# Kernel tuning notes

Measured on AMD Instinct MI355X. Metric: run time of the kernel, lower is better.

Reference implementation:

```python
import jax
import jax.numpy as jnp
import numpy as np

# Config mirroring GLOBAL_CONFIG['attn'] / kernel config in the source
BM = 64            # query-group (block) size; asserted 64 or 192 in source
TOP_KEYS = 0.1     # fraction of keys kept via top-k on colsum scores
MULTIPLE_OF = 64   # counts_multiple_of: indices_count rounded to this
LW1D = 0.15        # local_1d_window fraction
RAND_INV_PROB = 100

B, H, N, D = 1, 12, 2048, 128


def setup_inputs() -> dict:
    key = jax.random.key(0)
    kq, kk, kv, kc = jax.random.split(key, 4)
    shape = (B, H, N, D)
    q = jax.random.normal(kq, shape, dtype=jnp.float32)
    k = jax.random.normal(kk, shape, dtype=jnp.float32)
    v = jax.random.normal(kv, shape, dtype=jnp.float32)
    out_cache = jax.random.normal(kc, shape, dtype=jnp.float32)
    return {"q": q, "k": k, "v": v, "out_cache": out_cache}


def _static_1d_mask(n: int, bm: int, lw1d: float) -> jnp.ndarray:
    # initialize_1d_static_mask: per query-group local window centered at
    # qg*bm + bm//2, width int(lw1d*n), clipped to [0, n). Shape [qg, n].
    qg = n // bm
    ws = int(lw1d * n)
    centers = jnp.arange(qg) * bm + bm // 2          # [qg]
    j = jnp.arange(n)                                  # [n]
    lo = centers[:, None] - ws // 2
    hi = centers[:, None] + ws // 2
    return (j[None, :] >= lo) & (j[None, :] < hi)


def _scatter_true(mask, idx):
    # mask.scatter_(-1, idx, True) along last axis
    K = idx.shape[-1]
    n = mask.shape[-1]
    flat = mask.reshape(-1, n)
    fidx = idx.reshape(-1, K)
    rows = jnp.arange(flat.shape[0])[:, None]
    flat = flat.at[rows, fidx].set(True)
    return flat.reshape(mask.shape)


def _sparse_diff_attn(q, k, v, out_cache):
    b, h, n, d = q.shape
    qg = n // BM
    scale = 1.0 / jnp.sqrt(jnp.asarray(d, q.dtype))
    # dense scores (dense_colsum_attn computes these on the full step)
    scores = jnp.einsum('bhid,bhjd->bhij', q, k) * scale   # [b,h,n,n]
    probs = jax.nn.softmax(scores, axis=-1)
    # bs: column-sum of attention probabilities per query group  [b,h,qg,n]
    bs = probs.reshape(b, h, qg, BM, n).sum(axis=3)
    # indices_count = multiple_of * round(top_keys * n / multiple_of)
    indices_count = MULTIPLE_OF * int(round(TOP_KEYS * n / MULTIPLE_OF))
    rmask = jax.random.randint(jax.random.key(1), bs.shape, 0, RAND_INV_PROB) == 0
    _, idx = jax.lax.top_k(bs, indices_count)
    mask = _scatter_true(rmask, idx)                       # [b,h,qg,n]
    static = _static_1d_mask(n, BM, LW1D)                  # [qg,n]
    # video_query_groups: groups where static window + topk still sparse
    vqg = (static.sum(axis=-1, keepdims=True) + indices_count) < n  # [qg,1]
    mask = mask & vqg[None, None]
    mask = mask | static[None, None]
    # csp_attn: block-sparse attention; every query i in group i//BM attends
    # only to keys selected in mask[.., i//BM, :]
    full_mask = jnp.repeat(mask, BM, axis=2)               # [b,h,n,n]
    sp_scores = jnp.where(full_mask, scores, -jnp.inf)
    sp_probs = jax.nn.softmax(sp_scores, axis=-1)
    sp_out = jnp.einsum('bhij,bhjd->bhid', sp_probs, v)
    # sparse step: o = o_cache + csp_attn(...)  (sign = +1)
    return out_cache + sp_out


def reference(q, k, v, out_cache):
    return _sparse_diff_attn(q, k, v, out_cache)
```

## Files before the change

kernel.cpp:

```cpp
#include <hip/hip_runtime.h>
#include <math.h>

constexpr int Hh   = 12;
constexpr int Nn   = 2048;
constexpr int Dd   = 128;
constexpr int BMq  = 64;
constexpr int QGg  = 32;
constexpr int KSEL = 192;
constexpr int CK   = 32;
constexpr float SCALE = 0.08838834764831845f;

typedef _Float16 v8h __attribute__((ext_vector_type(8)));
typedef float    v4f __attribute__((ext_vector_type(4)));

__device__ __attribute__((aligned(16))) _Float16 g_qh[(size_t)Hh*Nn*Dd];
__device__ __attribute__((aligned(16))) _Float16 g_ql[(size_t)Hh*Nn*Dd];
__device__ __attribute__((aligned(16))) _Float16 g_kh[(size_t)Hh*Nn*Dd];
__device__ __attribute__((aligned(16))) _Float16 g_kl[(size_t)Hh*Nn*Dd];
__device__ float          g_lp[(size_t)Hh*Nn*16];
__device__ float          g_bs[(size_t)Hh*QGg*Nn];
__device__ unsigned short g_sel[Hh*QGg*Nn];
__device__ int            g_cnt[Hh*QGg];

__device__ __forceinline__ unsigned int rotl32(unsigned int x, int n){
  return (x << n) | (x >> (32 - n));
}

__device__ __forceinline__ unsigned pack2h(_Float16 a, _Float16 b){
  unsigned short ua, ub;
  __builtin_memcpy(&ua, &a, 2);
  __builtin_memcpy(&ub, &b, 2);
  return (unsigned)ua | ((unsigned)ub << 16);
}

__device__ __forceinline__ void tf2x32(unsigned int k0, unsigned int k1,
                                       unsigned int x0, unsigned int x1,
                                       unsigned int &o0, unsigned int &o1){
  const unsigned int ks2 = 0x1BD11BDAu ^ k0 ^ k1;
  x0 += k0; x1 += k1;
  x0 += x1; x1 = rotl32(x1,13); x1 ^= x0;
  x0 += x1; x1 = rotl32(x1,15); x1 ^= x0;
  x0 += x1; x1 = rotl32(x1,26); x1 ^= x0;
  x0 += x1; x1 = rotl32(x1, 6); x1 ^= x0;
  x0 += k1; x1 += ks2 + 1u;
  x0 += x1; x1 = rotl32(x1,17); x1 ^= x0;
  x0 += x1; x1 = rotl32(x1,29); x1 ^= x0;
  x0 += x1; x1 = rotl32(x1,16); x1 ^= x0;
  x0 += x1; x1 = rotl32(x1,24); x1 ^= x0;
  x0 += ks2; x1 += k0 + 2u;
  x0 += x1; x1 = rotl32(x1,13); x1 ^= x0;
  x0 += x1; x1 = rotl32(x1,15); x1 ^= x0;
  x0 += x1; x1 = rotl32(x1,26); x1 ^= x0;
  x0 += x1; x1 = rotl32(x1, 6); x1 ^= x0;
  x0 += k0; x1 += k1 + 3u;
  x0 += x1; x1 = rotl32(x1,17); x1 ^= x0;
  x0 += x1; x1 = rotl32(x1,29); x1 ^= x0;
  x0 += x1; x1 = rotl32(x1,16); x1 ^= x0;
  x0 += x1; x1 = rotl32(x1,24); x1 ^= x0;
  x0 += k1; x1 += ks2 + 4u;
  x0 += x1; x1 = rotl32(x1,13); x1 ^= x0;
  x0 += x1; x1 = rotl32(x1,15); x1 ^= x0;
  x0 += x1; x1 = rotl32(x1,26); x1 ^= x0;
  x0 += x1; x1 = rotl32(x1, 6); x1 ^= x0;
  x0 += ks2; x1 += k0 + 5u;
  o0 = x0; o1 = x1;
}

__device__ __forceinline__ bool jax_rand01(unsigned int idx,
                                           unsigned int k1a, unsigned int k1b,
                                           unsigned int k2a, unsigned int k2b){
  unsigned int h0, h1, l0, l1;
  tf2x32(k1a, k1b, 0u, idx, h0, h1);
  tf2x32(k2a, k2b, 0u, idx, l0, l1);
  unsigned int h = h0 ^ h1;
  unsigned int l = l0 ^ l1;
  unsigned int off = ((h % 100u) * 96u + (l % 100u)) % 100u;
  return off == 0u;
}

__global__ __launch_bounds__(256) void k0_cvt(const float* __restrict__ Q,
                                              const float* __restrict__ K){
  const int bid = blockIdx.x;
  const int t = threadIdx.x;
  const int kc = t >> 6, ln = t & 63;
  const int row = ln & 15;
  const int col = kc*32 + (ln >> 4)*8;
  const size_t src = ((size_t)bid*16 + row)*Dd + col;
  const size_t ob  = (((size_t)bid)*4 + kc)*512 + (size_t)ln*8;

  float4 qa = *(const float4*)(Q + src);
  float4 qb = *(const float4*)(Q + src + 4);
  float qs[8] = {qa.x*SCALE, qa.y*SCALE, qa.z*SCALE, qa.w*SCALE,
                 qb.x*SCALE, qb.y*SCALE, qb.z*SCALE, qb.w*SCALE};
  v8h qh, ql;
  #pragma unroll
  for (int j = 0; j < 8; ++j){
    _Float16 hi = (_Float16)qs[j];
    qh[j] = hi;
    ql[j] = (_Float16)(qs[j] - (float)hi);
  }
  *(v8h*)&g_qh[ob] = qh;
  *(v8h*)&g_ql[ob] = ql;

  float4 ka = *(const float4*)(K + src);
  float4 kb = *(const float4*)(K + src + 4);
  float ks[8] = {ka.x, ka.y, ka.z, ka.w, kb.x, kb.y, kb.z, kb.w};
  v8h kh, kl;
  #pragma unroll
  for (int j = 0; j < 8; ++j){
    _Float16 hi = (_Float16)ks[j];
    kh[j] = hi;
    kl[j] = (_Float16)(ks[j] - (float)hi);
  }
  *(v8h*)&g_kh[ob] = kh;
  *(v8h*)&g_kl[ob] = kl;
}

__global__ __launch_bounds__(256) void k1_rowsum(){
  const int bid0 = blockIdx.x;
  const int w = (bid0 & 7)*384 + (bid0 >> 3);
  const int jb = w & 15, gp = (w >> 4) & 15, h = w >> 8;
  const int t = threadIdx.x;
  const int wv = t >> 6, ln = t & 63;
  const int nidx = ln & 15, quad = ln >> 4;
  const size_t lnoff = (size_t)ln*8;
  const size_t habase = ((size_t)h*128 + gp*8 + wv*2)*4;
  const size_t hbbase = ((size_t)h*128 + jb*8)*4;

  __shared__ v8h Bh[2][8][64], Bl[2][8][64];
  const int f0 = t*2, f1 = t*2 + 1;
  const int tc0 = f0 >> 6, bln0 = f0 & 63;
  const int tc1 = f1 >> 6, bln1 = f1 & 63;

  v8h rbh0, rbh1, rbl0, rbl1;
  {
    const size_t a0 = (hbbase + tc0*4 + 0)*512 + (size_t)bln0*8;
    const size_t a1 = (hbbase + tc1*4 + 0)*512 + (size_t)bln1*8;
    rbh0 = *(const v8h*)&g_kh[a0]; rbh1 = *(const v8h*)&g_kh[a1];
    rbl0 = *(const v8h*)&g_kl[a0]; rbl1 = *(const v8h*)&g_kl[a1];
  }

  v4f acc[2][8];
  #pragma unroll
  for (int tr = 0; tr < 2; ++tr)
    #pragma unroll
    for (int tc = 0; tc < 8; ++tc)
      acc[tr][tc] = (v4f){0.f, 0.f, 0.f, 0.f};

  for (int kc = 0; kc < 4; ++kc){
    const int cur = kc & 1;
    Bh[cur][tc0][bln0] = rbh0; Bh[cur][tc1][bln1] = rbh1;
    Bl[cur][tc0][bln0] = rbl0; Bl[cur][tc1][bln1] = rbl1;
    __syncthreads();
    if (kc < 3){
      const size_t a0 = (hbbase + tc0*4 + kc+1)*512 + (size_t)bln0*8;
      const size_t a1 = (hbbase + tc1*4 + kc+1)*512 + (size_t)bln1*8;
      rbh0 = *(const v8h*)&g_kh[a0]; rbh1 = *(const v8h*)&g_kh[a1];
      rbl0 = *(const v8h*)&g_kl[a0]; rbl1 = *(const v8h*)&g_kl[a1];
    }
    v8h ahi[2], alo[2];
    #pragma unroll
    for (int tr = 0; tr < 2; ++tr){
      const size_t ab = (habase + tr*4 + kc)*512 + lnoff;
      ahi[tr] = *(const v8h*)&g_qh[ab];
      alo[tr] = *(const v8h*)&g_ql[ab];
    }
    #pragma unroll
    for (int tc = 0; tc < 8; ++tc){
      v8h bh = Bh[cur][tc][ln];
      v8h bl = Bl[cur][tc][ln];
      #pragma unroll
      for (int tr = 0; tr < 2; ++tr){
        acc[tr][tc] = __builtin_amdgcn_mfma_f32_16x16x32_f16(ahi[tr], bh, acc[tr][tc], 0, 0, 0);
        acc[tr][tc] = __builtin_amdgcn_mfma_f32_16x16x32_f16(ahi[tr], bl, acc[tr][tc], 0, 0, 0);
        acc[tr][tc] = __builtin_amdgcn_mfma_f32_16x16x32_f16(alo[tr], bh, acc[tr][tc], 0, 0, 0);
      }
    }
  }

  #pragma unroll
  for (int tr = 0; tr < 2; ++tr){
    float rs[4] = {0.f, 0.f, 0.f, 0.f};
    #pragma unroll
    for (int tc = 0; tc < 8; ++tc){
      #pragma unroll
      for (int r = 0; r < 4; ++r){
        rs[r] += __expf(acc[tr][tc][r]);
      }
    }
    #pragma unroll
    for (int r = 0; r < 4; ++r){
      float v = rs[r];
      v += __shfl_xor(v, 1);
      v += __shfl_xor(v, 2);
      v += __shfl_xor(v, 4);
      v += __shfl_xor(v, 8);
      rs[r] = v;
    }
    if (nidx == 0){
      #pragma unroll
      for (int r = 0; r < 4; ++r){
        const int row = (wv*2+tr)*16 + quad*4 + r;
        g_lp[((size_t)h*Nn + gp*128 + row)*16 + jb] = rs[r];
      }
    }
  }
}

__global__ __launch_bounds__(256) void k2r_colsum(){
  const int bid0 = blockIdx.x;
  const int w = (bid0 & 7)*384 + (bid0 >> 3);
  const int jb = w & 15, gp = (w >> 4) & 15, h = w >> 8;
  const int t = threadIdx.x;
  const int wv = t >> 6, ln = t & 63;
  const int nidx = ln & 15, quad = ln >> 4;
  const size_t lnoff = (size_t)ln*8;
  const size_t habase = ((size_t)h*128 + gp*8 + wv*2)*4;
  const size_t hbbase = ((size_t)h*128 + jb*8)*4;

  __shared__ v8h Bh[2][8][64], Bl[2][8][64];
  __shared__ float il_s[128];
  __shared__ float part[4][128];
  const int f0 = t*2, f1 = t*2 + 1;
  const int tc0 = f0 >> 6, bln0 = f0 & 63;
  const int tc1 = f1 >> 6, bln1 = f1 & 63;

  v8h rbh0, rbh1, rbl0, rbl1;
  {
    const size_t a0 = (hbbase + tc0*4 + 0)*512 + (size_t)bln0*8;
    const size_t a1 = (hbbase + tc1*4 + 0)*512 + (size_t)bln1*8;
    rbh0 = *(const v8h*)&g_kh[a0]; rbh1 = *(const v8h*)&g_kh[a1];
    rbl0 = *(const v8h*)&g_kl[a0]; rbl1 = *(const v8h*)&g_kl[a1];
  }
  if (t < 128){
    const float* lp = &g_lp[((size_t)h*Nn + gp*128 + t)*16];
    float s = 0.f;
    #pragma unroll
    for (int x = 0; x < 16; ++x) s += lp[x];
    il_s[t] = 1.0f / s;
  }

  v4f acc[2][8];
  #pragma unroll
  for (int tr = 0; tr < 2; ++tr)
    #pragma unroll
    for (int tc = 0; tc < 8; ++tc)
      acc[tr][tc] = (v4f){0.f, 0.f, 0.f, 0.f};

  for (int kc = 0; kc < 4; ++kc){
    const int cur = kc & 1;
    Bh[cur][tc0][bln0] = rbh0; Bh[cur][tc1][bln1] = rbh1;
    Bl[cur][tc0][bln0] = rbl0; Bl[cur][tc1][bln1] = rbl1;
    __syncthreads();
    if (kc < 3){
      const size_t a0 = (hbbase + tc0*4 + kc+1)*512 + (size_t)bln0*8;
      const size_t a1 = (hbbase + tc1*4 + kc+1)*512 + (size_t)bln1*8;
      rbh0 = *(const v8h*)&g_kh[a0]; rbh1 = *(const v8h*)&g_kh[a1];
      rbl0 = *(const v8h*)&g_kl[a0]; rbl1 = *(const v8h*)&g_kl[a1];
    }
    v8h ahi[2], alo[2];
    #pragma unroll
    for (int tr = 0; tr < 2; ++tr){
      const size_t ab = (habase + tr*4 + kc)*512 + lnoff;
      ahi[tr] = *(const v8h*)&g_qh[ab];
      alo[tr] = *(const v8h*)&g_ql[ab];
    }
    #pragma unroll
    for (int tc = 0; tc < 8; ++tc){
      v8h bh = Bh[cur][tc][ln];
      v8h bl = Bl[cur][tc][ln];
      #pragma unroll
      for (int tr = 0; tr < 2; ++tr){
        acc[tr][tc] = __builtin_amdgcn_mfma_f32_16x16x32_f16(ahi[tr], bh, acc[tr][tc], 0, 0, 0);
        acc[tr][tc] = __builtin_amdgcn_mfma_f32_16x16x32_f16(ahi[tr], bl, acc[tr][tc], 0, 0, 0);
        acc[tr][tc] = __builtin_amdgcn_mfma_f32_16x16x32_f16(alo[tr], bh, acc[tr][tc], 0, 0, 0);
      }
    }
  }

  __syncthreads();
  float csg[8];
  #pragma unroll
  for (int tc = 0; tc < 8; ++tc) csg[tc] = 0.f;
  #pragma unroll
  for (int tr = 0; tr < 2; ++tr){
    #pragma unroll
    for (int tc = 0; tc < 8; ++tc){
      float cs = 0.f;
      #pragma unroll
      for (int r = 0; r < 4; ++r){
        const int row = (wv*2+tr)*16 + quad*4 + r;
        cs += __expf(acc[tr][tc][r]) * il_s[row];
      }
      cs += __shfl_xor(cs, 16);
      cs += __shfl_xor(cs, 32);
      csg[tc] += cs;
    }
  }
  if (ln < 16){
    #pragma unroll
    for (int tc = 0; tc < 8; ++tc) part[wv][tc*16 + nidx] = csg[tc];
  }
  __syncthreads();
  const int col = t & 127, grp = t >> 7;
  g_bs[((size_t)h*QGg + gp*2 + grp)*Nn + jb*128 + col] =
      part[grp*2][col] + part[grp*2 + 1][col];
}

__global__ __launch_bounds__(256) void k2b_mask(){
  const int bid = blockIdx.x, g = bid % QGg, t = threadIdx.x;
  const int wv = t >> 6, lw = t & 63;
  __shared__ int hist[256];
  __shared__ int wsum[4];
  __shared__ int selb_s, selgt_s;
  __shared__ int csel;
  __shared__ int eqn;
  __shared__ int eqpos[Nn];
  const float* src = g_bs + (size_t)bid*Nn;
  float mine[8];
  {
    float4 a = *(const float4*)&src[t*4];
    float4 b = *(const float4*)&src[1024 + t*4];
    mine[0]=a.x; mine[1]=a.y; mine[2]=a.z; mine[3]=a.w;
    mine[4]=b.x; mine[5]=b.y; mine[6]=b.z; mine[7]=b.w;
  }
  if (t == 0){ csel = 0; eqn = 0; }
  unsigned int bu8[8];
  #pragma unroll
  for (int u = 0; u < 8; ++u) bu8[u] = __float_as_uint(mine[u]);

  unsigned int k1a, k1b, k2a, k2b;
  tf2x32(0u, 1u, 0u, 0u, k1a, k1b);
  tf2x32(0u, 1u, 0u, 1u, k2a, k2b);

  unsigned int pref = 0u;
  unsigned int msk  = 0u;
  int rem = KSEL;
  #pragma unroll
  for (int pass = 3; pass >= 0; --pass){
    const int shift = pass*8;
    hist[t] = 0;
    __syncthreads();
    #pragma unroll
    for (int u = 0; u < 8; ++u){
      if ((bu8[u] & msk) == pref)
        atomicAdd(&hist[(bu8[u] >> shift) & 0xFFu], 1);
    }
    __syncthreads();
    const int hcnt = hist[t];
    int s = hcnt;
    #pragma unroll
    for (int d = 1; d < 64; d <<= 1){
      int tmp = __shfl_down(s, d);
      if (lw + d < 64) s += tmp;
    }
    if (lw == 0) wsum[wv] = s;
    __syncthreads();
    int base = 0;
    #pragma unroll
    for (int w2 = 1; w2 < 4; ++w2) if (wv + w2 < 4) base += wsum[wv + w2];
    const int gt_incl = s + base;
    const int gt = gt_incl - hcnt;
    if (gt < rem && gt_incl >= rem){ selb_s = t; selgt_s = gt; }
    __syncthreads();
    pref |= ((unsigned)selb_s) << shift;
    msk  |= 0xFFu << shift;
    rem  -= selgt_s;
  }
  const unsigned int T = pref;
  const int need = rem;

  #pragma unroll
  for (int u = 0; u < 8; ++u){
    int j = (u < 4) ? (t*4 + u) : (1024 + t*4 + u - 4);
    if (bu8[u] == T){
      int s = atomicAdd(&eqn, 1);
      eqpos[s] = j;
    }
  }
  __syncthreads();
  const int en = eqn;

  const int lo = g*BMq + BMq/2 - 153;
  const int hi = g*BMq + BMq/2 + 153;
  const int ssum = ((hi < Nn) ? hi : Nn) - ((lo > 0) ? lo : 0);
  const bool vqg = (ssum + KSEL) < Nn;

  #pragma unroll
  for (int u = 0; u < 8; ++u){
    int j = (u < 4) ? (t*4 + u) : (1024 + t*4 + u - 4);
    unsigned int bu = bu8[u];
    bool topk = bu > T;
    if (!topk && bu == T){
      int tr = 0;
      for (int i = 0; i < en; ++i)
        tr += (eqpos[i] < j) ? 1 : 0;
      topk = (tr < need);
    }
    bool rnd = jax_rand01((unsigned)(bid*Nn + j), k1a, k1b, k2a, k2b);
    bool st  = (j >= lo) && (j < hi);
    bool selb = st || ((rnd || topk) && vqg);
    if (selb){
      int slot = atomicAdd(&csel, 1);
      g_sel[(size_t)bid*Nn + slot] = (unsigned short)j;
    }
  }
  __syncthreads();
  if (t == 0) g_cnt[bid] = csel;
}

__global__ __launch_bounds__(256) void k3_attn(const float* __restrict__ K,
                                               const float* __restrict__ V,
                                               const float* __restrict__ OC,
                                               float* __restrict__ out){
  const int bid0 = blockIdx.x;
  const int w    = (bid0 & 7)*96 + (bid0 >> 3);
  const int half = w & 1;
  const int gg   = w >> 1;
  const int h = gg / QGg, g = gg % QGg;
  const int t = threadIdx.x;
  const int wv = t >> 6, ln = t & 63;
  const int nidx = ln & 15, quad = ln >> 4;
  const int qtile = wv >> 1, kdt = wv & 1;

  __shared__ _Float16 kh_s[CK][136];
  __shared__ _Float16 kl_s[CK][136];
  __shared__ _Float16 vTh[Dd][40];
  __shared__ _Float16 vTl[Dd][40];
  __shared__ _Float16 p_h[32][40];
  __shared__ _Float16 p_l[32][40];
  __shared__ float    l_part[2][32];
  __shared__ float    l_s[32];

  const int c = g_cnt[gg];
  const unsigned short* sel = g_sel + (size_t)gg*Nn;

  const int rb = g*4 + half*2 + qtile;
  v8h aHi[4], aLo[4];
  #pragma unroll
  for (int kc = 0; kc < 4; ++kc){
    const size_t ab = (((size_t)h*128 + rb)*4 + kc)*512 + (size_t)ln*8;
    aHi[kc] = *(const v8h*)&g_qh[ab];
    aLo[kc] = *(const v8h*)&g_ql[ab];
  }

  if (t < 64) l_part[t >> 5][t & 31] = 0.0f;

  float4 kreg[4], vreg[4];
  {
    const int cc0 = (c < CK) ? c : CK;
    #pragma unroll
    for (int it = 0; it < 4; ++it){
      int e = it*256 + t, row = e >> 5, c4 = e & 31;
      int j = (row < cc0) ? (int)sel[row] : 0;
      kreg[it] = ((const float4*)(K + ((size_t)h*Nn + j)*Dd))[c4];
      vreg[it] = ((const float4*)(V + ((size_t)h*Nn + j)*Dd))[c4];
    }
  }

  v4f acc[4];
  #pragma unroll
  for (int dt = 0; dt < 4; ++dt) acc[dt] = (v4f){0.f, 0.f, 0.f, 0.f};

  const int cg = (quad ^ ((nidx >> 2) & 3)) * 8;

  for (int c0 = 0; c0 < c; c0 += CK){
    const int cc = ((c - c0) < CK) ? (c - c0) : CK;
    #pragma unroll
    for (int it = 0; it < 4; ++it){
      int e = it*256 + t, row = e >> 5, c4 = e & 31;
      float4 kv = kreg[it];
      float xs[4] = {kv.x, kv.y, kv.z, kv.w};
      _Float16 hh[4], ll[4];
      #pragma unroll
      for (int m = 0; m < 4; ++m){
        _Float16 hi = (_Float16)xs[m];
        hh[m] = hi;
        ll[m] = (_Float16)(xs[m] - (float)hi);
      }
      *(unsigned*)&kh_s[row][c4*4 + 0] = pack2h(hh[0], hh[1]);
      *(unsigned*)&kh_s[row][c4*4 + 2] = pack2h(hh[2], hh[3]);
      *(unsigned*)&kl_s[row][c4*4 + 0] = pack2h(ll[0], ll[1]);
      *(unsigned*)&kl_s[row][c4*4 + 2] = pack2h(ll[2], ll[3]);
      float4 vv = vreg[it];
      float vs[4] = {vv.x, vv.y, vv.z, vv.w};
      const int swz = row ^ ((c4 & 3) << 3);
      #pragma unroll
      for (int m = 0; m < 4; ++m){
        _Float16 hi = (_Float16)vs[m];
        vTh[c4*4 + m][swz] = hi;
        vTl[c4*4 + m][swz] = (_Float16)(vs[m] - (float)hi);
      }
    }
    __syncthreads();
    {
      const int nc0 = c0 + CK;
      if (nc0 < c){
        const int ncc = ((c - nc0) < CK) ? (c - nc0) : CK;
        #pragma unroll
        for (int it = 0; it < 4; ++it){
          int e = it*256 + t, row = e >> 5, c4 = e & 31;
          int j = (row < ncc) ? (int)sel[nc0 + row] : 0;
          kreg[it] = ((const float4*)(K + ((size_t)h*Nn + j)*Dd))[c4];
          vreg[it] = ((const float4*)(V + ((size_t)h*Nn + j)*Dd))[c4];
        }
      }
    }
    v4f sc = (v4f){0.f, 0.f, 0.f, 0.f};
    #pragma unroll
    for (int kc = 0; kc < 4; ++kc){
      v8h bh = *(const v8h*)&kh_s[kdt*16 + nidx][kc*32 + quad*8];
      v8h bl = *(const v8h*)&kl_s[kdt*16 + nidx][kc*32 + quad*8];
      sc = __builtin_amdgcn_mfma_f32_16x16x32_f16(aHi[kc], bh, sc, 0, 0, 0);
      sc = __builtin_amdgcn_mfma_f32_16x16x32_f16(aHi[kc], bl, sc, 0, 0, 0);
      sc = __builtin_amdgcn_mfma_f32_16x16x32_f16(aLo[kc], bh, sc, 0, 0, 0);
    }
    {
      const int k_loc = kdt*16 + nidx;
      float rs[4];
      #pragma unroll
      for (int r = 0; r < 4; ++r){
        float sv = (k_loc < cc) ? __expf(sc[r]) : 0.f;
        rs[r] = sv;
        _Float16 hi = (_Float16)sv;
        const int row = qtile*16 + quad*4 + r;
        p_h[row][k_loc] = hi;
        p_l[row][k_loc] = (_Float16)(sv - (float)hi);
      }
      #pragma unroll
      for (int r = 0; r < 4; ++r){
        float v = rs[r];
        v += __shfl_xor(v, 1);
        v += __shfl_xor(v, 2);
        v += __shfl_xor(v, 4);
        v += __shfl_xor(v, 8);
        rs[r] = v;
      }
      if (nidx == 0){
        #pragma unroll
        for (int r = 0; r < 4; ++r)
          l_part[kdt][qtile*16 + quad*4 + r] += rs[r];
      }
    }
    __syncthreads();
    {
      v8h ph = *(const v8h*)&p_h[qtile*16 + nidx][quad*8];
      v8h pl = *(const v8h*)&p_l[qtile*16 + nidx][quad*8];
      #pragma unroll
      for (int dt = 0; dt < 4; ++dt){
        const int d = (kdt*4 + dt)*16 + nidx;
        v8h vh = *(const v8h*)&vTh[d][cg];
        v8h vl = *(const v8h*)&vTl[d][cg];
        acc[dt] = __builtin_amdgcn_mfma_f32_16x16x32_f16(ph, vh, acc[dt], 0, 0, 0);
        acc[dt] = __builtin_amdgcn_mfma_f32_16x16x32_f16(ph, vl, acc[dt], 0, 0, 0);
        acc[dt] = __builtin_amdgcn_mfma_f32_16x16x32_f16(pl, vh, acc[dt], 0, 0, 0);
      }
    }
    __syncthreads();
  }

  if (t < 32) l_s[t] = 1.0f / (l_part[0][t] + l_part[1][t]);
  __syncthreads();

  #pragma unroll
  for (int dt = 0; dt < 4; ++dt){
    const int d = (kdt*4 + dt)*16 + nidx;
    #pragma unroll
    for (int r = 0; r < 4; ++r){
      const int row = qtile*16 + quad*4 + r;
      const float il = l_s[row];
      const size_t o = ((size_t)h*Nn + (size_t)g*BMq + half*32 + row)*Dd + d;
      out[o] = acc[dt][r]*il + OC[o];
    }
  }
}

extern "C" void kernel_launch(void* const* d_in, const int* in_sizes, int n_in,
                              void* d_out, int out_size, void* d_ws, size_t ws_size,
                              hipStream_t stream) {
  (void)in_sizes; (void)n_in; (void)out_size; (void)d_ws; (void)ws_size;
  const float* Q  = (const float*)d_in[0];
  const float* K  = (const float*)d_in[1];
  const float* V  = (const float*)d_in[2];
  const float* OC = (const float*)d_in[3];
  float* out = (float*)d_out;
  hipLaunchKernelGGL(k0_cvt,     dim3(Hh*128),   dim3(256), 0, stream, Q, K);
  hipLaunchKernelGGL(k1_rowsum,  dim3(Hh*16*16), dim3(256), 0, stream);
  hipLaunchKernelGGL(k2r_colsum, dim3(Hh*16*16), dim3(256), 0, stream);
  hipLaunchKernelGGL(k2b_mask,   dim3(Hh*QGg),   dim3(256), 0, stream);
  hipLaunchKernelGGL(k3_attn,    dim3(Hh*QGg*2), dim3(256), 0, stream, K, V, OC, out);
}
```

Baseline: 262.4 us.

## Split sparse attention key range across two blocks and combine partials

The sparse attention kernel now splits each query block's selected-key list into two halves processed by separate workgroups, doubling the grid from 768 to 1536 blocks. Each writes unnormalized partial outputs and row sums to global scratch. A new combine kernel sums the partials, normalizes, and adds the output cache. This is meant to raise occupancy and parallelism on the GPU, at the cost of an extra launch and a round trip of partial results through global memory. It works without per-split max rescaling because the existing code appears to accumulate raw exp sums.

```diff
diff --git a/kernel.cpp b/kernel.cpp
--- a/kernel.cpp
+++ b/kernel.cpp
@@ -21,6 +21,8 @@
 __device__ float          g_bs[(size_t)Hh*QGg*Nn];
 __device__ unsigned short g_sel[Hh*QGg*Nn];
 __device__ int            g_cnt[Hh*QGg];
+__device__ __attribute__((aligned(16))) float g_oacc[(size_t)Hh*QGg*2*2*32*128];
+__device__ float          g_lacc[(size_t)Hh*QGg*2*2*32];
 
 __device__ __forceinline__ unsigned int rotl32(unsigned int x, int n){
   return (x << n) | (x >> (32 - n));
@@ -410,13 +412,13 @@
 }
 
 __global__ __launch_bounds__(256) void k3_attn(const float* __restrict__ K,
-                                               const float* __restrict__ V,
-                                               const float* __restrict__ OC,
-                                               float* __restrict__ out){
+                                               const float* __restrict__ V){
   const int bid0 = blockIdx.x;
-  const int w    = (bid0 & 7)*96 + (bid0 >> 3);
-  const int half = w & 1;
-  const int gg   = w >> 1;
+  const int w    = (bid0 & 7)*192 + (bid0 >> 3);
+  const int ks   = w & 1;
+  const int pb   = w >> 1;
+  const int half = pb & 1;
+  const int gg   = pb >> 1;
   const int h = gg / QGg, g = gg % QGg;
   const int t = threadIdx.x;
   const int wv = t >> 6, ln = t & 63;
@@ -430,10 +432,13 @@
   __shared__ _Float16 p_h[32][40];
   __shared__ _Float16 p_l[32][40];
   __shared__ float    l_part[2][32];
-  __shared__ float    l_s[32];
 
   const int c = g_cnt[gg];
   const unsigned short* sel = g_sel + (size_t)gg*Nn;
+  const int nch = (c + CK - 1) / CK;
+  const int ch  = ((nch + 1) / 2) * CK;
+  const int cbeg = ks * ch;
+  const int cend = (c < cbeg + ch) ? c : (cbeg + ch);
 
   const int rb = g*4 + half*2 + qtile;
   v8h aHi[4], aLo[4];
@@ -447,12 +452,12 @@
   if (t < 64) l_part[t >> 5][t & 31] = 0.0f;
 
   float4 kreg[4], vreg[4];
-  {
-    const int cc0 = (c < CK) ? c : CK;
+  if (cbeg < cend){
+    const int cc0 = ((cend - cbeg) < CK) ? (cend - cbeg) : CK;
     #pragma unroll
     for (int it = 0; it < 4; ++it){
       int e = it*256 + t, row = e >> 5, c4 = e & 31;
-      int j = (row < cc0) ? (int)sel[row] : 0;
+      int j = (row < cc0) ? (int)sel[cbeg + row] : 0;
       kreg[it] = ((const float4*)(K + ((size_t)h*Nn + j)*Dd))[c4];
       vreg[it] = ((const float4*)(V + ((size_t)h*Nn + j)*Dd))[c4];
     }
@@ -464,8 +469,8 @@
 
   const int cg = (quad ^ ((nidx >> 2) & 3)) * 8;
 
-  for (int c0 = 0; c0 < c; c0 += CK){
-    const int cc = ((c - c0) < CK) ? (c - c0) : CK;
+  for (int c0 = cbeg; c0 < cend; c0 += CK){
+    const int cc = ((cend - c0) < CK) ? (cend - c0) : CK;
     #pragma unroll
     for (int it = 0; it < 4; ++it){
       int e = it*256 + t, row = e >> 5, c4 = e & 31;
@@ -495,8 +500,8 @@
     __syncthreads();
     {
       const int nc0 = c0 + CK;
-      if (nc0 < c){
-        const int ncc = ((c - nc0) < CK) ? (c - nc0) : CK;
+      if (nc0 < cend){
+        const int ncc = ((cend - nc0) < CK) ? (cend - nc0) : CK;
         #pragma unroll
         for (int it = 0; it < 4; ++it){
           int e = it*256 + t, row = e >> 5, c4 = e & 31;
@@ -559,19 +564,51 @@
     __syncthreads();
   }
 
-  if (t < 32) l_s[t] = 1.0f / (l_part[0][t] + l_part[1][t]);
   __syncthreads();
-
+  const size_t pbase = ((size_t)pb*2 + ks)*4096;
+  if (t < 32) g_lacc[((size_t)pb*2 + ks)*32 + t] = l_part[0][t] + l_part[1][t];
   #pragma unroll
   for (int dt = 0; dt < 4; ++dt){
     const int d = (kdt*4 + dt)*16 + nidx;
     #pragma unroll
     for (int r = 0; r < 4; ++r){
       const int row = qtile*16 + quad*4 + r;
-      const float il = l_s[row];
-      const size_t o = ((size_t)h*Nn + (size_t)g*BMq + half*32 + row)*Dd + d;
-      out[o] = acc[dt][r]*il + OC[o];
-    }
+      g_oacc[pbase + (size_t)row*128 + d] = acc[dt][r];
+    }
+  }
+}
+
+__global__ __launch_bounds__(256) void k4_comb(const float* __restrict__ OC,
+                                               float* __restrict__ out){
+  const int pb = blockIdx.x;
+  const int half = pb & 1;
+  const int gg = pb >> 1;
+  const int h = gg / QGg, g = gg % QGg;
+  const int t = threadIdx.x;
+  __shared__ float il_s[32];
+  if (t < 32){
+    float l0 = g_lacc[((size_t)pb*2 + 0)*32 + t];
+    float l1 = g_lacc[((size_t)pb*2 + 1)*32 + t];
+    il_s[t] = 1.0f / (l0 + l1);
+  }
+  __syncthreads();
+  const size_t b0 = ((size_t)pb*2 + 0)*4096;
+  const size_t b1 = ((size_t)pb*2 + 1)*4096;
+  #pragma unroll
+  for (int i = 0; i < 4; ++i){
+    int e = i*256 + t;
+    int row = e >> 5, c4 = e & 31;
+    float4 a0 = *(const float4*)&g_oacc[b0 + (size_t)row*128 + c4*4];
+    float4 a1 = *(const float4*)&g_oacc[b1 + (size_t)row*128 + c4*4];
+    const float il = il_s[row];
+    const size_t o = ((size_t)h*Nn + (size_t)g*BMq + half*32 + row)*Dd + c4*4;
+    float4 oc = *(const float4*)(OC + o);
+    float4 rr;
+    rr.x = (a0.x + a1.x)*il + oc.x;
+    rr.y = (a0.y + a1.y)*il + oc.y;
+    rr.z = (a0.z + a1.z)*il + oc.z;
+    rr.w = (a0.w + a1.w)*il + oc.w;
+    *(float4*)(out + o) = rr;
   }
 }
 
@@ -584,9 +621,10 @@
   const float* V  = (const float*)d_in[2];
   const float* OC = (const float*)d_in[3];
   float* out = (float*)d_out;
-  hipLaunchKernelGGL(k0_cvt,     dim3(Hh*128),   dim3(256), 0, stream, Q, K);
-  hipLaunchKernelGGL(k1_rowsum,  dim3(Hh*16*16), dim3(256), 0, stream);
-  hipLaunchKernelGGL(k2r_colsum, dim3(Hh*16*16), dim3(256), 0, stream);
-  hipLaunchKernelGGL(k2b_mask,   dim3(Hh*QGg),   dim3(256), 0, stream);
-  hipLaunchKernelGGL(k3_attn,    dim3(Hh*QGg*2), dim3(256), 0, stream, K, V, OC, out);
-}
+  hipLaunchKernelGGL(k0_cvt,     dim3(Hh*128),     dim3(256), 0, stream, Q, K);
+  hipLaunchKernelGGL(k1_rowsum,  dim3(Hh*16*16),   dim3(256), 0, stream);
+  hipLaunchKernelGGL(k2r_colsum, dim3(Hh*16*16),   dim3(256), 0, stream);
+  hipLaunchKernelGGL(k2b_mask,   dim3(Hh*QGg),     dim3(256), 0, stream);
+  hipLaunchKernelGGL(k3_attn,    dim3(Hh*QGg*2*2), dim3(256), 0, stream, K, V);
+  hipLaunchKernelGGL(k4_comb,    dim3(Hh*QGg*2),   dim3(256), 0, stream, OC, out);
+}
```

After: 267.9 us. +2.1%, slower.
